# Kernel optimization log

Measured on AMD Instinct MI355X. Metric: run time of the kernel, lower is better.

Reference implementation:

```python
import jax, jax.numpy as jnp
import numpy as np

N = 50000      # nodes
E = 800000     # edges
D = 64         # model dim (in_dim == out_dim)
H = 8          # heads
Dh = D // H    # head dim = 8
CLAMP = 5.0
EPS_BN = 1e-5


def setup_inputs() -> dict:
    key = jax.random.key(0)
    ks = jax.random.split(key, 16)
    g = lambda i, shape, s=0.1: (jax.random.normal(ks[i], shape, jnp.float32) * s)
    z = lambda shape: jnp.zeros(shape, jnp.float32)
    o = lambda shape: jnp.ones(shape, jnp.float32)
    return dict(
        x=g(0, (N, D), 1.0),
        edge_attr=g(1, (E, D), 1.0),
        edge_index=jax.random.randint(ks[2], (2, E), 0, N, jnp.int32),
        Wq=g(3, (D, H * Dh)), bq=z((H * Dh,)),
        Wk=g(4, (D, H * Dh)),                      # K: use_bias=False (cfg default)
        We=g(5, (D, 2 * H * Dh)), be=z((2 * H * Dh,)),
        Wv=g(6, (D, H * Dh)),                      # V: use_bias=False
        Aw=g(7, (Dh, H, 1)),
        VeRow=g(8, (Dh, H, Dh)),
        deg_coef=g(9, (1, D, 2)),
        WOh=g(10, (D, D)), bOh=z((D,)),
        WOe=g(11, (D, D)), bOe=z((D,)),
        gamma1h=o((D,)), beta1h=z((D,)),
        gamma1e=o((D,)), beta1e=z((D,)),
        W1=g(12, (D, 2 * D)), b1=z((2 * D,)),
        W2=g(13, (2 * D, D)), b2=z((D,)),
        gamma2h=o((D,)), beta2h=z((D,)),
    )


def _bn(v, gamma, beta):
    # BatchNorm1d with batch statistics (training-mode math, biased var as in torch)
    mu = v.mean(axis=0)
    var = ((v - mu) ** 2).mean(axis=0)
    return (v - mu) * jax.lax.rsqrt(var + EPS_BN) * gamma + beta


def reference(x, edge_attr, edge_index, Wq, bq, Wk, We, be, Wv, Aw, VeRow,
              deg_coef, WOh, bOh, WOe, bOe, gamma1h, beta1h, gamma1e, beta1e,
              W1, b1, W2, b2, gamma2h, beta2h):
    src, dst = edge_index[0], edge_index[1]
    # degree scaler: deg computed on the fly from edge_index[1]
    deg = jax.ops.segment_sum(jnp.ones((E,), x.dtype), dst, num_segments=N)
    log_deg = jnp.log(deg + 1.0)[:, None]                       # [N,1]

    Q = (x @ Wq + bq).reshape(N, H, Dh)
    K = (x @ Wk).reshape(N, H, Dh)
    V = (x @ Wv).reshape(N, H, Dh)
    Ee = (edge_attr @ We + be).reshape(E, H, 2 * Dh)
    Ew, Eb = Ee[:, :, :Dh], Ee[:, :, Dh:]

    s = (K[src] + Q[dst]) * Ew                                  # [E,H,Dh]
    s = jnp.sqrt(jax.nn.relu(s)) - jnp.sqrt(jax.nn.relu(-s))    # signed sqrt
    s = jax.nn.relu(s + Eb)                                     # attn act = relu
    e_t = s
    wE = s.reshape(E, H * Dh)

    score = jnp.einsum('ehd,dhc->ehc', s, Aw)                   # [E,H,1]
    score = jnp.clip(score, -CLAMP, CLAMP)
    # segment softmax over destination nodes
    m = jax.ops.segment_max(score, dst, num_segments=N)
    m = jnp.where(jnp.isfinite(m), m, 0.0)
    ex = jnp.exp(score - m[dst])
    denom = jax.ops.segment_sum(ex, dst, num_segments=N)
    attn = ex / (denom[dst] + 1e-16)                            # [E,H,1]

    wV = jax.ops.segment_sum(V[src] * attn, dst, num_segments=N)    # [N,H,Dh]
    rowV = jax.ops.segment_sum(e_t * attn, dst, num_segments=N)     # [N,H,Dh]
    wV = wV + jnp.einsum('nhd,dhc->nhc', rowV, VeRow)

    h = wV.reshape(N, H * Dh)
    h = h * deg_coef[:, :, 0] + (h * log_deg) * deg_coef[:, :, 1]
    h = h @ WOh + bOh
    e = wE @ WOe + bOe

    h = _bn(x + h, gamma1h, beta1h)
    e = _bn(edge_attr + e, gamma1e, beta1e)

    h2 = jax.nn.relu(h @ W1 + b1) @ W2 + b2
    h = _bn(h + h2, gamma2h, beta2h)
    return h, e
```

## Files before the change

kernel.cpp:

```cpp
#include <hip/hip_runtime.h>
#include <hip/hip_bf16.h>

#define N_NODES 50000
#define N_EDGES 800000
#define CLAMP_V 5.0f
#define MAXDEG 64

typedef __hip_bfloat16 bf16;

__device__ __forceinline__ float b2f(bf16 v){ return __bfloat162float(v); }
__device__ __forceinline__ bf16 f2b(float v){ return __float2bfloat16(v); }

__device__ __forceinline__ float ldin(const void* p, size_t i, bool f32){
  return f32 ? ((const float*)p)[i] : b2f(((const bf16*)p)[i]);
}
__device__ __forceinline__ void stout(void* p, size_t i, float v, bool f32){
  if(f32) ((float*)p)[i]=v; else ((bf16*)p)[i]=f2b(v);
}
__device__ __forceinline__ void* e_region(void* d_out, bool f32){
  return f32 ? (void*)((float*)d_out + (size_t)N_NODES*64)
             : (void*)((bf16*)d_out + (size_t)N_NODES*64);
}

#define W_FLAG 0
#define W_DEG  64
#define W_ST   50064
#define W_ZEND 50448
#define W_BUCK 50448
#define W_QK   3250448
#define W_V    9650448
#define W_HV   12850448
#define W_END  16050448
#define W_HPRE W_QK
#define W_HSUM W_BUCK

__global__ void detect_kernel(const unsigned short* __restrict__ wq_raw, unsigned* __restrict__ flag){
  int t=threadIdx.x; int cnt=0;
  for(int i=t;i<4096;i+=64){
    unsigned e=(wq_raw[i]>>7)&0xFF;
    if(e>=130) cnt++;
  }
  for(int o=32;o;o>>=1) cnt+=__shfl_down(cnt,o);
  if(t==0) *flag = (cnt>64)? 1u:0u;
}

__global__ __launch_bounds__(256) void build_kernel(const int* __restrict__ edge_index,
    unsigned* __restrict__ deg, unsigned* __restrict__ bucket)
{
  int e = blockIdx.x*256+threadIdx.x;
  if(e < N_EDGES){
    int dst = edge_index[N_EDGES+e];
    unsigned j = atomicAdd(&deg[dst],1u);
    if(j < MAXDEG) bucket[(size_t)dst*MAXDEG + j] = (unsigned)e;
  }
}

__global__ __launch_bounds__(256) void qkv_kernel(const void* __restrict__ x,
    const void* __restrict__ Wq, const void* __restrict__ bq,
    const void* __restrict__ Wk, const void* __restrict__ Wv,
    const unsigned* __restrict__ flagp, float* __restrict__ qk, float* __restrict__ vbuf)
{
  const bool f = (*flagp)!=0;
  __shared__ float sW[64*192];
  __shared__ float4 sxT[4][64];
  int t=threadIdx.x, wave=t>>6, lane=t&63;
  for (int i=t;i<64*64;i+=256){ int k=i>>6, j=i&63;
    sW[k*192+j]=ldin(Wq,i,f); sW[k*192+64+j]=ldin(Wk,i,f); sW[k*192+128+j]=ldin(Wv,i,f); }
  float bqv = ldin(bq,lane,f);
  __syncthreads();
  const int groups = N_NODES/16;
  for (int g=blockIdx.x; g<groups; g+=gridDim.x){
    int n0 = g*16 + wave*4;
    float v0=ldin(x,(size_t)(n0+0)*64+lane,f);
    float v1=ldin(x,(size_t)(n0+1)*64+lane,f);
    float v2=ldin(x,(size_t)(n0+2)*64+lane,f);
    float v3=ldin(x,(size_t)(n0+3)*64+lane,f);
    sxT[wave][lane]=make_float4(v0,v1,v2,v3);
    float aq[4]={0,0,0,0}, ak[4]={0,0,0,0}, av[4]={0,0,0,0};
    #pragma unroll 8
    for(int k=0;k<64;k++){
      float4 a = sxT[wave][k];
      float w0=sW[k*192+lane], w1=sW[k*192+64+lane], w2=sW[k*192+128+lane];
      aq[0]+=a.x*w0; aq[1]+=a.y*w0; aq[2]+=a.z*w0; aq[3]+=a.w*w0;
      ak[0]+=a.x*w1; ak[1]+=a.y*w1; ak[2]+=a.z*w1; ak[3]+=a.w*w1;
      av[0]+=a.x*w2; av[1]+=a.y*w2; av[2]+=a.z*w2; av[3]+=a.w*w2;
    }
    #pragma unroll
    for(int r=0;r<4;r++){
      int n=n0+r;
      qk[n*128+lane]     = aq[r]+bqv;
      qk[n*128+64+lane]  = ak[r];
      vbuf[n*64+lane]    = av[r];
    }
  }
}

__global__ __launch_bounds__(256) void edgeA_kernel(
    const void* __restrict__ edge_attr, const int* __restrict__ edge_index,
    const void* __restrict__ We, const void* __restrict__ be,
    const float* __restrict__ qk, const unsigned* __restrict__ flagp, void* __restrict__ d_out)
{
  const bool f = (*flagp)!=0;
  void* s_buf = e_region(d_out,f);
  __shared__ float sWW[64*64], sWB[64*64];
  __shared__ float4 seaT[4][64];
  int t=threadIdx.x, wave=t>>6, lane=t&63;
  int h=lane>>3, d=lane&7;
  for(int i=t;i<64*64;i+=256){ int k=i>>6, c=i&63; int hh=c>>3, dd=c&7;
    sWW[i]=ldin(We,(size_t)k*128+hh*16+dd,f);
    sWB[i]=ldin(We,(size_t)k*128+hh*16+8+dd,f); }
  float beW=ldin(be,h*16+d,f), beB=ldin(be,h*16+8+d,f);
  __syncthreads();
  const int groups = N_EDGES/16;
  for(int g=blockIdx.x; g<groups; g+=gridDim.x){
    int e0 = g*16 + wave*4;
    float v0=ldin(edge_attr,(size_t)(e0+0)*64+lane,f);
    float v1=ldin(edge_attr,(size_t)(e0+1)*64+lane,f);
    float v2=ldin(edge_attr,(size_t)(e0+2)*64+lane,f);
    float v3=ldin(edge_attr,(size_t)(e0+3)*64+lane,f);
    seaT[wave][lane]=make_float4(v0,v1,v2,v3);
    float aW[4]={0,0,0,0}, aB[4]={0,0,0,0};
    #pragma unroll 8
    for(int k=0;k<64;k++){
      float4 a=seaT[wave][k];
      float wW=sWW[k*64+lane], wB=sWB[k*64+lane];
      aW[0]+=a.x*wW; aW[1]+=a.y*wW; aW[2]+=a.z*wW; aW[3]+=a.w*wW;
      aB[0]+=a.x*wB; aB[1]+=a.y*wB; aB[2]+=a.z*wB; aB[3]+=a.w*wB;
    }
    #pragma unroll
    for(int r=0;r<4;r++){
      int e=e0+r;
      int src=edge_index[e], dst=edge_index[N_EDGES+e];
      float Ew = aW[r]+beW;
      float Eb = aB[r]+beB;
      float kq = qk[src*128+64+lane] + qk[dst*128+lane];
      float s1 = kq*Ew;
      float ss = (s1>=0.f) ? sqrtf(s1) : -sqrtf(-s1);
      float s2 = ss+Eb; s2 = s2>0.f ? s2 : 0.f;
      stout(s_buf,(size_t)e*64+lane,s2,f);
    }
  }
}

__global__ __launch_bounds__(256) void gather_kernel(
    const unsigned* __restrict__ deg, const unsigned* __restrict__ bucket,
    const int* __restrict__ edge_index,
    const void* __restrict__ Aw, const void* __restrict__ VeRow, const void* __restrict__ deg_coef,
    const float* __restrict__ vbuf, const unsigned* __restrict__ flagp,
    void* __restrict__ d_out, float* __restrict__ hv)
{
  const bool f = (*flagp)!=0;
  const void* s_buf = e_region(d_out,f);
  int t=threadIdx.x, wave=t>>6, lane=t&63;
  int h=lane>>3, d=lane&7;
  float awv = ldin(Aw, d*8+h, f);
  float ver[8];
  #pragma unroll
  for(int dd=0;dd<8;dd++) ver[dd]=ldin(VeRow,(dd*8+h)*8+d,f);
  float dc0=ldin(deg_coef,lane*2,f), dc1=ldin(deg_coef,lane*2+1,f);

  int n = blockIdx.x*4 + wave;
  unsigned degree = deg[n];
  int len = (int)(degree < MAXDEG ? degree : MAXDEG);
  const unsigned* bk = &bucket[(size_t)n*MAXDEG];

  float m=-1e30f, den=0.f, wv=0.f, rv=0.f;
  unsigned en; int srcn;
  if(len>0){ en = bk[0]; srcn = edge_index[en]; }
  for(int j=0;j<len;j++){
    unsigned e = en; int src = srcn;
    if(j+1<len){ en = bk[j+1]; srcn = edge_index[en]; }
    float sval = ldin(s_buf,(size_t)e*64+lane,f);
    float vv   = vbuf[src*64+lane];
    float p = sval*awv;
    p += __shfl_xor(p,1);
    p += __shfl_xor(p,2);
    p += __shfl_xor(p,4);
    p = fminf(fmaxf(p,-CLAMP_V),CLAMP_V);
    float nm = fmaxf(m,p);
    float sc = __expf(m-nm);
    float ex = __expf(p-nm);
    den = den*sc + ex;
    wv  = wv*sc  + vv*ex;
    rv  = rv*sc  + sval*ex;
    m = nm;
  }
  float inv = 1.f/(den + 1e-16f);
  wv *= inv; rv *= inv;
  float rvp=0.f;
  #pragma unroll
  for(int dd=0;dd<8;dd++){
    float rvd = __shfl(rv, (lane & 56) + dd);
    rvp += rvd * ver[dd];
  }
  float ld = __logf((float)degree + 1.f);
  hv[(size_t)n*64+lane] = (wv + rvp) * (dc0 + ld*dc1);
}

__global__ __launch_bounds__(256) void edgeD_kernel(const void* __restrict__ edge_attr,
    const void* __restrict__ WOe, const void* __restrict__ bOe,
    const unsigned* __restrict__ flagp, void* __restrict__ d_out, float* __restrict__ stats)
{
  const bool f = (*flagp)!=0;
  void* e_io = e_region(d_out,f);
  __shared__ float sW[64*64];
  __shared__ float4 sTa[4][64], sTb[4][64];
  int t=threadIdx.x, wave=t>>6, lane=t&63;
  for(int i=t;i<64*64;i+=256) sW[i]=ldin(WOe,i,f);
  float bo=ldin(bOe,lane,f);
  float s1=0.f,s2=0.f;
  __syncthreads();
  const int groups=N_EDGES/32;
  for(int g=blockIdx.x;g<groups;g+=gridDim.x){
    int e0=g*32+wave*8;
    float v[8];
    #pragma unroll
    for(int r=0;r<8;r++) v[r]=ldin(e_io,(size_t)(e0+r)*64+lane,f);
    sTa[wave][lane]=make_float4(v[0],v[1],v[2],v[3]);
    sTb[wave][lane]=make_float4(v[4],v[5],v[6],v[7]);
    float acc[8]={0,0,0,0,0,0,0,0};
    #pragma unroll 8
    for(int k=0;k<64;k++){
      float4 a=sTa[wave][k], b=sTb[wave][k];
      float w=sW[k*64+lane];
      acc[0]+=a.x*w; acc[1]+=a.y*w; acc[2]+=a.z*w; acc[3]+=a.w*w;
      acc[4]+=b.x*w; acc[5]+=b.y*w; acc[6]+=b.z*w; acc[7]+=b.w*w;
    }
    #pragma unroll
    for(int r=0;r<8;r++){
      int e=e0+r;
      float ep=ldin(edge_attr,(size_t)e*64+lane,f)+bo+acc[r];
      stout(e_io,(size_t)e*64+lane,ep,f);
      s1+=ep; s2+=ep*ep;
    }
  }
  atomicAdd(&stats[lane], s1);
  atomicAdd(&stats[64+lane], s2);
}

__global__ __launch_bounds__(256) void edgeE_kernel(const unsigned* __restrict__ flagp,
    void* __restrict__ d_out, const float* __restrict__ stats,
    const void* __restrict__ g1e, const void* __restrict__ b1e)
{
  const bool f = (*flagp)!=0;
  void* e_io = e_region(d_out,f);
  size_t tid=(size_t)blockIdx.x*256+threadIdx.x;
  int c=(int)(tid&63);
  float mu=stats[c]*(1.f/N_EDGES);
  float var=stats[64+c]*(1.f/N_EDGES)-mu*mu;
  float rs=rsqrtf(var+1e-5f);
  float val=ldin(e_io,tid,f);
  val=(val-mu)*rs*ldin(g1e,c,f)+ldin(b1e,c,f);
  stout(e_io,tid,val,f);
}

__global__ __launch_bounds__(256) void h1_kernel(const float* __restrict__ hv,
    const void* __restrict__ WOh, const void* __restrict__ bOh, const void* __restrict__ x,
    const unsigned* __restrict__ flagp, float* __restrict__ hpre, float* __restrict__ stats)
{
  const bool f = (*flagp)!=0;
  __shared__ float sW[64*64];
  __shared__ float4 sT[4][64];
  int t=threadIdx.x, wave=t>>6, lane=t&63;
  for(int i=t;i<64*64;i+=256) sW[i]=ldin(WOh,i,f);
  float bo=ldin(bOh,lane,f);
  float s1=0.f,s2=0.f;
  __syncthreads();
  const int groups=N_NODES/16;
  for(int g=blockIdx.x;g<groups;g+=gridDim.x){
    int n0=g*16+wave*4;
    sT[wave][lane]=make_float4(hv[(n0+0)*64+lane],hv[(n0+1)*64+lane],
                               hv[(n0+2)*64+lane],hv[(n0+3)*64+lane]);
    float acc[4]={0,0,0,0};
    #pragma unroll 8
    for(int k=0;k<64;k++){
      float4 a=sT[wave][k]; float w=sW[k*64+lane];
      acc[0]+=a.x*w; acc[1]+=a.y*w; acc[2]+=a.z*w; acc[3]+=a.w*w;
    }
    #pragma unroll
    for(int r=0;r<4;r++){
      int n=n0+r;
      float hp=ldin(x,(size_t)n*64+lane,f)+bo+acc[r];
      hpre[n*64+lane]=hp;
      s1+=hp; s2+=hp*hp;
    }
  }
  atomicAdd(&stats[128+lane],s1);
  atomicAdd(&stats[192+lane],s2);
}

__global__ __launch_bounds__(256) void h2_kernel(const float* __restrict__ hpre,
    const void* __restrict__ W1, const void* __restrict__ b1, const void* __restrict__ W2, const void* __restrict__ b2,
    const void* __restrict__ g1h, const void* __restrict__ be1h,
    const unsigned* __restrict__ flagp, float* __restrict__ hsum, float* __restrict__ stats)
{
  const bool f = (*flagp)!=0;
  __shared__ float sW1[64*128];
  __shared__ float4 shT[4][64];
  __shared__ float4 stT[4][128];
  int t=threadIdx.x, wave=t>>6, lane=t&63;
  for(int i=t;i<64*128;i+=256) sW1[i]=ldin(W1,i,f);
  float mu=stats[128+lane]*(1.f/N_NODES);
  float var=stats[192+lane]*(1.f/N_NODES)-mu*mu;
  float rs=rsqrtf(var+1e-5f);
  float gg=ldin(g1h,lane,f), bb=ldin(be1h,lane,f);
  float b1a=ldin(b1,lane,f), b1b=ldin(b1,64+lane,f);
  float b2c=ldin(b2,lane,f);
  float s1=0.f,s2=0.f;
  __syncthreads();
  const int groups=N_NODES/16;
  for(int g=blockIdx.x;g<groups;g+=gridDim.x){
    int n0=g*16+wave*4;
    float h1v[4];
    #pragma unroll
    for(int r=0;r<4;r++) h1v[r]=(hpre[(n0+r)*64+lane]-mu)*rs*gg+bb;
    shT[wave][lane]=make_float4(h1v[0],h1v[1],h1v[2],h1v[3]);
    float t0[4]={0,0,0,0}, t1[4]={0,0,0,0};
    #pragma unroll 8
    for(int k=0;k<64;k++){
      float4 a=shT[wave][k];
      float w0=sW1[k*128+lane], w1=sW1[k*128+64+lane];
      t0[0]+=a.x*w0; t0[1]+=a.y*w0; t0[2]+=a.z*w0; t0[3]+=a.w*w0;
      t1[0]+=a.x*w1; t1[1]+=a.y*w1; t1[2]+=a.z*w1; t1[3]+=a.w*w1;
    }
    #pragma unroll
    for(int r=0;r<4;r++){ t0[r]=fmaxf(t0[r]+b1a,0.f); t1[r]=fmaxf(t1[r]+b1b,0.f); }
    stT[wave][lane]=make_float4(t0[0],t0[1],t0[2],t0[3]);
    stT[wave][64+lane]=make_float4(t1[0],t1[1],t1[2],t1[3]);
    float acc[4]={0,0,0,0};
    #pragma unroll 8
    for(int k=0;k<128;k++){
      float4 a=stT[wave][k];
      float w=ldin(W2,(size_t)k*64+lane,f);
      acc[0]+=a.x*w; acc[1]+=a.y*w; acc[2]+=a.z*w; acc[3]+=a.w*w;
    }
    #pragma unroll
    for(int r=0;r<4;r++){
      float hs=h1v[r]+acc[r]+b2c;
      hsum[(n0+r)*64+lane]=hs;
      s1+=hs; s2+=hs*hs;
    }
  }
  atomicAdd(&stats[256+lane],s1);
  atomicAdd(&stats[320+lane],s2);
}

__global__ __launch_bounds__(256) void h3_kernel(const float* __restrict__ hsum,
    const float* __restrict__ stats, const void* __restrict__ g2h, const void* __restrict__ b2h,
    const unsigned* __restrict__ flagp, void* __restrict__ d_out)
{
  const bool f = (*flagp)!=0;
  int tid=blockIdx.x*256+threadIdx.x;
  int c=tid&63;
  float mu=stats[256+c]*(1.f/N_NODES);
  float var=stats[320+c]*(1.f/N_NODES)-mu*mu;
  float rs=rsqrtf(var+1e-5f);
  float val=(hsum[tid]-mu)*rs*ldin(g2h,c,f)+ldin(b2h,c,f);
  stout(d_out,tid,val,f);
}

extern "C" void kernel_launch(void* const* d_in, const int* in_sizes, int n_in,
                              void* d_out, int out_size, void* d_ws, size_t ws_size,
                              hipStream_t stream)
{
  const void* x        =d_in[0];
  const void* edge_attr=d_in[1];
  const int*  edge_index=(const int*)d_in[2];
  const void* Wq =d_in[3];
  const void* bq =d_in[4];
  const void* Wk =d_in[5];
  const void* We =d_in[6];
  const void* be =d_in[7];
  const void* Wv =d_in[8];
  const void* Aw =d_in[9];
  const void* VeRow=d_in[10];
  const void* deg_coef=d_in[11];
  const void* WOh=d_in[12];
  const void* bOh=d_in[13];
  const void* WOe=d_in[14];
  const void* bOe=d_in[15];
  const void* g1h=d_in[16];
  const void* be1h=d_in[17];
  const void* g1e=d_in[18];
  const void* be1e=d_in[19];
  const void* W1 =d_in[20];
  const void* b1 =d_in[21];
  const void* W2 =d_in[22];
  const void* b2 =d_in[23];
  const void* g2h=d_in[24];
  const void* be2h=d_in[25];

  float* ws=(float*)d_ws;
  unsigned* flag  =(unsigned*)(ws+W_FLAG);
  unsigned* deg   =(unsigned*)(ws+W_DEG);
  unsigned* bucket=(unsigned*)(ws+W_BUCK);
  float* stats=ws+W_ST;
  float* qk   =ws+W_QK;
  float* vbuf =ws+W_V;
  float* hv   =ws+W_HV;
  float* hpre =ws+W_HPRE;
  float* hsum =ws+W_HSUM;

  hipMemsetAsync(d_ws,0,(size_t)W_ZEND*4,stream);
  hipLaunchKernelGGL(detect_kernel,dim3(1),dim3(64),0,stream,(const unsigned short*)Wq,flag);
  hipLaunchKernelGGL(build_kernel, dim3(3125), dim3(256),0,stream, edge_index,deg,bucket);
  hipLaunchKernelGGL(qkv_kernel,   dim3(1024), dim3(256),0,stream, x,Wq,bq,Wk,Wv,flag,qk,vbuf);
  hipLaunchKernelGGL(edgeA_kernel, dim3(1024), dim3(256),0,stream, edge_attr,edge_index,We,be,qk,flag,d_out);
  hipLaunchKernelGGL(gather_kernel,dim3(12500),dim3(256),0,stream, deg,bucket,edge_index,Aw,VeRow,deg_coef,vbuf,flag,d_out,hv);
  hipLaunchKernelGGL(edgeD_kernel, dim3(1024), dim3(256),0,stream, edge_attr,WOe,bOe,flag,d_out,stats);
  hipLaunchKernelGGL(edgeE_kernel, dim3(200000),dim3(256),0,stream, flag,d_out,stats,g1e,be1e);
  hipLaunchKernelGGL(h1_kernel,    dim3(1024), dim3(256),0,stream, hv,WOh,bOh,x,flag,hpre,stats);
  hipLaunchKernelGGL(h2_kernel,    dim3(1024), dim3(256),0,stream, hpre,W1,b1,W2,b2,g1h,be1h,flag,hsum,stats);
  hipLaunchKernelGGL(h3_kernel,    dim3(12500),dim3(256),0,stream, hsum,stats,g2h,be2h,flag,d_out);
}
```

Baseline: 1.599 ms.

## Use bf16 MFMA for edge projections and batch gather with fixed-max softmax

For bf16 inputs, the edge projection (edge_attr@We) and the output projection (wE@WOe) now use 16x16x32 bf16 MFMA instructions with swizzled LDS-staged weights held in registers, replacing scalar FMA loops. The BN statistics are reduced in LDS before the global atomics. The bucket now stores (edge, src) pairs so the gather skips the dependent edge_index lookup. The gather processes four edges per step and uses the clamp bound as a fixed softmax max instead of an online running max, which removes the rescaling exps. Workspace offsets are reshuffled to fit the wider bucket. Risks: the fixed max relies on scores being clamped to [-5,5], and the fp32 path is left unchanged.

Measured after the change: 1.546 ms. 3.3% less time.

```diff
diff --git a/kernel.cpp b/kernel.cpp
--- a/kernel.cpp
+++ b/kernel.cpp
@@ -7,6 +7,8 @@
 #define MAXDEG 64
 
 typedef __hip_bfloat16 bf16;
+typedef short s16x8 __attribute__((ext_vector_type(8)));
+typedef float f32x4 __attribute__((ext_vector_type(4)));
 
 __device__ __forceinline__ float b2f(bf16 v){ return __bfloat162float(v); }
 __device__ __forceinline__ bf16 f2b(float v){ return __float2bfloat16(v); }
@@ -27,12 +29,12 @@
 #define W_ST   50064
 #define W_ZEND 50448
 #define W_BUCK 50448
-#define W_QK   3250448
-#define W_V    9650448
-#define W_HV   12850448
+#define W_QK   6450448
+#define W_V    12850448
 #define W_END  16050448
-#define W_HPRE W_QK
-#define W_HSUM W_BUCK
+#define W_HV   W_QK
+#define W_HPRE W_BUCK
+#define W_HSUM (W_BUCK+3200000)
 
 __global__ void detect_kernel(const unsigned short* __restrict__ wq_raw, unsigned* __restrict__ flag){
   int t=threadIdx.x; int cnt=0;
@@ -45,13 +47,14 @@
 }
 
 __global__ __launch_bounds__(256) void build_kernel(const int* __restrict__ edge_index,
-    unsigned* __restrict__ deg, unsigned* __restrict__ bucket)
+    unsigned* __restrict__ deg, uint2* __restrict__ buck2)
 {
   int e = blockIdx.x*256+threadIdx.x;
   if(e < N_EDGES){
+    int src = edge_index[e];
     int dst = edge_index[N_EDGES+e];
     unsigned j = atomicAdd(&deg[dst],1u);
-    if(j < MAXDEG) bucket[(size_t)dst*MAXDEG + j] = (unsigned)e;
+    if(j < MAXDEG) buck2[(size_t)dst*MAXDEG + j] = make_uint2((unsigned)e,(unsigned)src);
   }
 }
 
@@ -101,50 +104,120 @@
     const float* __restrict__ qk, const unsigned* __restrict__ flagp, void* __restrict__ d_out)
 {
   const bool f = (*flagp)!=0;
-  void* s_buf = e_region(d_out,f);
-  __shared__ float sWW[64*64], sWB[64*64];
-  __shared__ float4 seaT[4][64];
+  __shared__ float4 sm4[2304];
+  float* sm=(float*)sm4;
   int t=threadIdx.x, wave=t>>6, lane=t&63;
-  int h=lane>>3, d=lane&7;
-  for(int i=t;i<64*64;i+=256){ int k=i>>6, c=i&63; int hh=c>>3, dd=c&7;
-    sWW[i]=ldin(We,(size_t)k*128+hh*16+dd,f);
-    sWB[i]=ldin(We,(size_t)k*128+hh*16+8+dd,f); }
-  float beW=ldin(be,h*16+d,f), beB=ldin(be,h*16+8+d,f);
-  __syncthreads();
-  const int groups = N_EDGES/16;
-  for(int g=blockIdx.x; g<groups; g+=gridDim.x){
-    int e0 = g*16 + wave*4;
-    float v0=ldin(edge_attr,(size_t)(e0+0)*64+lane,f);
-    float v1=ldin(edge_attr,(size_t)(e0+1)*64+lane,f);
-    float v2=ldin(edge_attr,(size_t)(e0+2)*64+lane,f);
-    float v3=ldin(edge_attr,(size_t)(e0+3)*64+lane,f);
-    seaT[wave][lane]=make_float4(v0,v1,v2,v3);
-    float aW[4]={0,0,0,0}, aB[4]={0,0,0,0};
-    #pragma unroll 8
-    for(int k=0;k<64;k++){
-      float4 a=seaT[wave][k];
-      float wW=sWW[k*64+lane], wB=sWB[k*64+lane];
-      aW[0]+=a.x*wW; aW[1]+=a.y*wW; aW[2]+=a.z*wW; aW[3]+=a.w*wW;
-      aB[0]+=a.x*wB; aB[1]+=a.y*wB; aB[2]+=a.z*wB; aB[3]+=a.w*wB;
-    }
-    #pragma unroll
-    for(int r=0;r<4;r++){
-      int e=e0+r;
-      int src=edge_index[e], dst=edge_index[N_EDGES+e];
-      float Ew = aW[r]+beW;
-      float Eb = aB[r]+beB;
-      float kq = qk[src*128+64+lane] + qk[dst*128+lane];
-      float s1 = kq*Ew;
-      float ss = (s1>=0.f) ? sqrtf(s1) : -sqrtf(-s1);
-      float s2 = ss+Eb; s2 = s2>0.f ? s2 : 0.f;
-      stout(s_buf,(size_t)e*64+lane,s2,f);
+  if(!f){
+    bf16* s_out = (bf16*)d_out + (size_t)N_NODES*64;
+    const unsigned short* ea = (const unsigned short*)edge_attr;
+    unsigned short* BT = (unsigned short*)sm;
+    for(int i=t;i<128*64;i+=256){
+      int j=i>>6, k=i&63; int jj=j&63;
+      int colW = ((jj>>3)<<4) + ((j>>6)<<3) + (jj&7);
+      BT[(j*128 + ((k*2)^((j&7)<<4)))>>1] = ((const unsigned short*)We)[(size_t)k*128+colW];
+    }
+    __syncthreads();
+    int qg=lane>>4, col=lane&15;
+    s16x8 Bf[8][2];
+    #pragma unroll
+    for(int tl=0;tl<8;tl++){
+      int j=tl*16+col;
+      #pragma unroll
+      for(int q=0;q<2;q++){
+        int kb=qg*8+q*32;
+        Bf[tl][q] = *(const s16x8*)((const char*)BT + j*128 + ((kb*2)^((j&7)<<4)));
+      }
+    }
+    float beWv[4], beBv[4];
+    #pragma unroll
+    for(int tl=0;tl<4;tl++){
+      int c=tl*16+col;
+      beWv[tl]=b2f(((const bf16*)be)[((c>>3)<<4)+(c&7)]);
+      beBv[tl]=b2f(((const bf16*)be)[((c>>3)<<4)+8+(c&7)]);
+    }
+    f32x4 zz; zz[0]=0.f; zz[1]=0.f; zz[2]=0.f; zz[3]=0.f;
+    const int groups = N_EDGES/64;
+    for(int g=blockIdx.x; g<groups; g+=gridDim.x){
+      int e0=g*64+wave*16;
+      int eq=e0+qg*4;
+      int srcs[4],dsts[4];
+      #pragma unroll
+      for(int r=0;r<4;r++){ srcs[r]=edge_index[eq+r]; dsts[r]=edge_index[N_EDGES+eq+r]; }
+      const unsigned short* ap = ea + (size_t)(e0+col)*64 + qg*8;
+      s16x8 A0 = *(const s16x8*)ap;
+      s16x8 A1 = *(const s16x8*)(ap+32);
+      float kqv[4][4];
+      #pragma unroll
+      for(int r=0;r<4;r++){
+        #pragma unroll
+        for(int tl=0;tl<4;tl++){
+          int c=tl*16+col;
+          kqv[r][tl] = qk[(size_t)srcs[r]*128+64+c] + qk[(size_t)dsts[r]*128+c];
+        }
+      }
+      f32x4 acc[8];
+      #pragma unroll
+      for(int tl=0;tl<8;tl++){
+        acc[tl]=__builtin_amdgcn_mfma_f32_16x16x32_bf16(A0,Bf[tl][0],zz,0,0,0);
+        acc[tl]=__builtin_amdgcn_mfma_f32_16x16x32_bf16(A1,Bf[tl][1],acc[tl],0,0,0);
+      }
+      #pragma unroll
+      for(int r=0;r<4;r++){
+        size_t eo=(size_t)(eq+r)*64;
+        #pragma unroll
+        for(int tl=0;tl<4;tl++){
+          float Ew=acc[tl][r]+beWv[tl];
+          float Eb=acc[tl+4][r]+beBv[tl];
+          float s1v=kqv[r][tl]*Ew;
+          float ssv=(s1v>=0.f)?sqrtf(s1v):-sqrtf(-s1v);
+          float s2v=ssv+Eb; s2v=s2v>0.f?s2v:0.f;
+          s_out[eo+tl*16+col]=f2b(s2v);
+        }
+      }
+    }
+  } else {
+    void* s_buf = e_region(d_out,f);
+    float* sWW=sm; float* sWB=sm+4096; float4* seaT=(float4*)(sm+8192);
+    int h=lane>>3, d=lane&7;
+    for(int i=t;i<64*64;i+=256){ int k=i>>6, c=i&63; int hh=c>>3, dd=c&7;
+      sWW[i]=ldin(We,(size_t)k*128+hh*16+dd,f);
+      sWB[i]=ldin(We,(size_t)k*128+hh*16+8+dd,f); }
+    float beW=ldin(be,h*16+d,f), beB=ldin(be,h*16+8+d,f);
+    __syncthreads();
+    const int groups = N_EDGES/16;
+    for(int g=blockIdx.x; g<groups; g+=gridDim.x){
+      int e0 = g*16 + wave*4;
+      float v0=ldin(edge_attr,(size_t)(e0+0)*64+lane,f);
+      float v1=ldin(edge_attr,(size_t)(e0+1)*64+lane,f);
+      float v2=ldin(edge_attr,(size_t)(e0+2)*64+lane,f);
+      float v3=ldin(edge_attr,(size_t)(e0+3)*64+lane,f);
+      seaT[wave*64+lane]=make_float4(v0,v1,v2,v3);
+      float aW[4]={0,0,0,0}, aB[4]={0,0,0,0};
+      #pragma unroll 8
+      for(int k=0;k<64;k++){
+        float4 a=seaT[wave*64+k];
+        float wW=sWW[k*64+lane], wB=sWB[k*64+lane];
+        aW[0]+=a.x*wW; aW[1]+=a.y*wW; aW[2]+=a.z*wW; aW[3]+=a.w*wW;
+        aB[0]+=a.x*wB; aB[1]+=a.y*wB; aB[2]+=a.z*wB; aB[3]+=a.w*wB;
+      }
+      #pragma unroll
+      for(int r=0;r<4;r++){
+        int e=e0+r;
+        int src=edge_index[e], dst=edge_index[N_EDGES+e];
+        float Ew = aW[r]+beW;
+        float Eb = aB[r]+beB;
+        float kq = qk[src*128+64+lane] + qk[dst*128+lane];
+        float s1 = kq*Ew;
+        float ss = (s1>=0.f) ? sqrtf(s1) : -sqrtf(-s1);
+        float s2 = ss+Eb; s2 = s2>0.f ? s2 : 0.f;
+        stout(s_buf,(size_t)e*64+lane,s2,f);
+      }
     }
   }
 }
 
 __global__ __launch_bounds__(256) void gather_kernel(
-    const unsigned* __restrict__ deg, const unsigned* __restrict__ bucket,
-    const int* __restrict__ edge_index,
+    const unsigned* __restrict__ deg, const uint2* __restrict__ buck2,
     const void* __restrict__ Aw, const void* __restrict__ VeRow, const void* __restrict__ deg_coef,
     const float* __restrict__ vbuf, const unsigned* __restrict__ flagp,
     void* __restrict__ d_out, float* __restrict__ hv)
@@ -162,28 +235,29 @@
   int n = blockIdx.x*4 + wave;
   unsigned degree = deg[n];
   int len = (int)(degree < MAXDEG ? degree : MAXDEG);
-  const unsigned* bk = &bucket[(size_t)n*MAXDEG];
-
-  float m=-1e30f, den=0.f, wv=0.f, rv=0.f;
-  unsigned en; int srcn;
-  if(len>0){ en = bk[0]; srcn = edge_index[en]; }
-  for(int j=0;j<len;j++){
-    unsigned e = en; int src = srcn;
-    if(j+1<len){ en = bk[j+1]; srcn = edge_index[en]; }
-    float sval = ldin(s_buf,(size_t)e*64+lane,f);
-    float vv   = vbuf[src*64+lane];
-    float p = sval*awv;
-    p += __shfl_xor(p,1);
-    p += __shfl_xor(p,2);
-    p += __shfl_xor(p,4);
-    p = fminf(fmaxf(p,-CLAMP_V),CLAMP_V);
-    float nm = fmaxf(m,p);
-    float sc = __expf(m-nm);
-    float ex = __expf(p-nm);
-    den = den*sc + ex;
-    wv  = wv*sc  + vv*ex;
-    rv  = rv*sc  + sval*ex;
-    m = nm;
+  const uint2* bk = &buck2[(size_t)n*MAXDEG];
+
+  float den=0.f, wv=0.f, rv=0.f;
+  for(int j=0;j<len;j+=4){
+    float sv[4], vq[4]; int valid[4];
+    #pragma unroll
+    for(int i=0;i<4;i++){
+      int jj=j+i; int js = jj<len ? jj : len-1;
+      uint2 es = bk[js];
+      sv[i]=ldin(s_buf,(size_t)es.x*64+lane,f);
+      vq[i]=vbuf[(size_t)es.y*64+lane];
+      valid[i]=(jj<len);
+    }
+    #pragma unroll
+    for(int i=0;i<4;i++){
+      float p = sv[i]*awv;
+      p += __shfl_xor(p,1);
+      p += __shfl_xor(p,2);
+      p += __shfl_xor(p,4);
+      p = fminf(fmaxf(p,-CLAMP_V),CLAMP_V);
+      float ex = valid[i] ? __expf(p-CLAMP_V) : 0.f;
+      den += ex; wv += vq[i]*ex; rv += sv[i]*ex;
+    }
   }
   float inv = 1.f/(den + 1e-16f);
   wv *= inv; rv *= inv;
@@ -202,40 +276,102 @@
     const unsigned* __restrict__ flagp, void* __restrict__ d_out, float* __restrict__ stats)
 {
   const bool f = (*flagp)!=0;
-  void* e_io = e_region(d_out,f);
-  __shared__ float sW[64*64];
-  __shared__ float4 sTa[4][64], sTb[4][64];
+  __shared__ float4 sm4[1536];
+  float* sm=(float*)sm4;
   int t=threadIdx.x, wave=t>>6, lane=t&63;
-  for(int i=t;i<64*64;i+=256) sW[i]=ldin(WOe,i,f);
-  float bo=ldin(bOe,lane,f);
-  float s1=0.f,s2=0.f;
-  __syncthreads();
-  const int groups=N_EDGES/32;
-  for(int g=blockIdx.x;g<groups;g+=gridDim.x){
-    int e0=g*32+wave*8;
-    float v[8];
-    #pragma unroll
-    for(int r=0;r<8;r++) v[r]=ldin(e_io,(size_t)(e0+r)*64+lane,f);
-    sTa[wave][lane]=make_float4(v[0],v[1],v[2],v[3]);
-    sTb[wave][lane]=make_float4(v[4],v[5],v[6],v[7]);
-    float acc[8]={0,0,0,0,0,0,0,0};
-    #pragma unroll 8
-    for(int k=0;k<64;k++){
-      float4 a=sTa[wave][k], b=sTb[wave][k];
-      float w=sW[k*64+lane];
-      acc[0]+=a.x*w; acc[1]+=a.y*w; acc[2]+=a.z*w; acc[3]+=a.w*w;
-      acc[4]+=b.x*w; acc[5]+=b.y*w; acc[6]+=b.z*w; acc[7]+=b.w*w;
-    }
-    #pragma unroll
-    for(int r=0;r<8;r++){
-      int e=e0+r;
-      float ep=ldin(edge_attr,(size_t)e*64+lane,f)+bo+acc[r];
-      stout(e_io,(size_t)e*64+lane,ep,f);
-      s1+=ep; s2+=ep*ep;
-    }
-  }
-  atomicAdd(&stats[lane], s1);
-  atomicAdd(&stats[64+lane], s2);
+  if(!f){
+    bf16* eio = (bf16*)d_out + (size_t)N_NODES*64;
+    const unsigned short* sb=(const unsigned short*)eio;
+    unsigned short* BT=(unsigned short*)sm;
+    float* red = sm + 2048;
+    if(t<128) red[t]=0.f;
+    for(int i=t;i<4096;i+=256){
+      int j=i>>6, k=i&63;
+      BT[(j*128+((k*2)^((j&7)<<4)))>>1]=((const unsigned short*)WOe)[(size_t)k*64+j];
+    }
+    __syncthreads();
+    int qg=lane>>4, col=lane&15;
+    s16x8 Bf[4][2];
+    #pragma unroll
+    for(int tl=0;tl<4;tl++){
+      int j=tl*16+col;
+      #pragma unroll
+      for(int q=0;q<2;q++){
+        int kb=qg*8+q*32;
+        Bf[tl][q]=*(const s16x8*)((const char*)BT+j*128+((kb*2)^((j&7)<<4)));
+      }
+    }
+    float boV[4];
+    #pragma unroll
+    for(int tl=0;tl<4;tl++) boV[tl]=b2f(((const bf16*)bOe)[tl*16+col]);
+    float st1[4]={0,0,0,0}, st2[4]={0,0,0,0};
+    f32x4 zz; zz[0]=0.f; zz[1]=0.f; zz[2]=0.f; zz[3]=0.f;
+    const int groups=N_EDGES/64;
+    for(int g=blockIdx.x; g<groups; g+=gridDim.x){
+      int e0=g*64+wave*16, eq=e0+qg*4;
+      const unsigned short* apr = sb + (size_t)(e0+col)*64 + qg*8;
+      s16x8 A0=*(const s16x8*)apr;
+      s16x8 A1=*(const s16x8*)(apr+32);
+      f32x4 acc[4];
+      #pragma unroll
+      for(int tl=0;tl<4;tl++){
+        acc[tl]=__builtin_amdgcn_mfma_f32_16x16x32_bf16(A0,Bf[tl][0],zz,0,0,0);
+        acc[tl]=__builtin_amdgcn_mfma_f32_16x16x32_bf16(A1,Bf[tl][1],acc[tl],0,0,0);
+      }
+      #pragma unroll
+      for(int r=0;r<4;r++){
+        size_t eo=(size_t)(eq+r)*64;
+        #pragma unroll
+        for(int tl=0;tl<4;tl++){
+          int c=tl*16+col;
+          float ep=b2f(((const bf16*)edge_attr)[eo+c])+boV[tl]+acc[tl][r];
+          eio[eo+c]=f2b(ep);
+          st1[tl]+=ep; st2[tl]+=ep*ep;
+        }
+      }
+    }
+    #pragma unroll
+    for(int tl=0;tl<4;tl++){
+      int c=tl*16+col;
+      atomicAdd(&red[c],st1[tl]);
+      atomicAdd(&red[64+c],st2[tl]);
+    }
+    __syncthreads();
+    if(t<128) atomicAdd(&stats[t],red[t]);
+  } else {
+    void* e_io = e_region(d_out,f);
+    float* sW=sm; float4* sTa=(float4*)(sm+4096); float4* sTb=(float4*)(sm+5120);
+    for(int i=t;i<64*64;i+=256) sW[i]=ldin(WOe,i,f);
+    float bo=ldin(bOe,lane,f);
+    float s1=0.f,s2=0.f;
+    __syncthreads();
+    const int groups=N_EDGES/32;
+    for(int g=blockIdx.x;g<groups;g+=gridDim.x){
+      int e0=g*32+wave*8;
+      float v[8];
+      #pragma unroll
+      for(int r=0;r<8;r++) v[r]=ldin(e_io,(size_t)(e0+r)*64+lane,f);
+      sTa[wave*64+lane]=make_float4(v[0],v[1],v[2],v[3]);
+      sTb[wave*64+lane]=make_float4(v[4],v[5],v[6],v[7]);
+      float acc[8]={0,0,0,0,0,0,0,0};
+      #pragma unroll 8
+      for(int k=0;k<64;k++){
+        float4 a=sTa[wave*64+k], b=sTb[wave*64+k];
+        float w=sW[k*64+lane];
+        acc[0]+=a.x*w; acc[1]+=a.y*w; acc[2]+=a.z*w; acc[3]+=a.w*w;
+        acc[4]+=b.x*w; acc[5]+=b.y*w; acc[6]+=b.z*w; acc[7]+=b.w*w;
+      }
+      #pragma unroll
+      for(int r=0;r<8;r++){
+        int e=e0+r;
+        float ep=ldin(edge_attr,(size_t)e*64+lane,f)+bo+acc[r];
+        stout(e_io,(size_t)e*64+lane,ep,f);
+        s1+=ep; s2+=ep*ep;
+      }
+    }
+    atomicAdd(&stats[lane], s1);
+    atomicAdd(&stats[64+lane], s2);
+  }
 }
 
 __global__ __launch_bounds__(256) void edgeE_kernel(const unsigned* __restrict__ flagp,
@@ -393,7 +529,7 @@
   float* ws=(float*)d_ws;
   unsigned* flag  =(unsigned*)(ws+W_FLAG);
   unsigned* deg   =(unsigned*)(ws+W_DEG);
-  unsigned* bucket=(unsigned*)(ws+W_BUCK);
+  uint2*    buck2 =(uint2*)(ws+W_BUCK);
   float* stats=ws+W_ST;
   float* qk   =ws+W_QK;
   float* vbuf =ws+W_V;
@@ -403,10 +539,10 @@
 
   hipMemsetAsync(d_ws,0,(size_t)W_ZEND*4,stream);
   hipLaunchKernelGGL(detect_kernel,dim3(1),dim3(64),0,stream,(const unsigned short*)Wq,flag);
-  hipLaunchKernelGGL(build_kernel, dim3(3125), dim3(256),0,stream, edge_index,deg,bucket);
+  hipLaunchKernelGGL(build_kernel, dim3(3125), dim3(256),0,stream, edge_index,deg,buck2);
   hipLaunchKernelGGL(qkv_kernel,   dim3(1024), dim3(256),0,stream, x,Wq,bq,Wk,Wv,flag,qk,vbuf);
   hipLaunchKernelGGL(edgeA_kernel, dim3(1024), dim3(256),0,stream, edge_attr,edge_index,We,be,qk,flag,d_out);
-  hipLaunchKernelGGL(gather_kernel,dim3(12500),dim3(256),0,stream, deg,bucket,edge_index,Aw,VeRow,deg_coef,vbuf,flag,d_out,hv);
+  hipLaunchKernelGGL(gather_kernel,dim3(12500),dim3(256),0,stream, deg,buck2,Aw,VeRow,deg_coef,vbuf,flag,d_out,hv);
   hipLaunchKernelGGL(edgeD_kernel, dim3(1024), dim3(256),0,stream, edge_attr,WOe,bOe,flag,d_out,stats);
   hipLaunchKernelGGL(edgeE_kernel, dim3(200000),dim3(256),0,stream, flag,d_out,stats,g1e,be1e);
   hipLaunchKernelGGL(h1_kernel,    dim3(1024), dim3(256),0,stream, hv,WOh,bOh,x,flag,hpre,stats);
```
